# Optimization experiments

Measured on AMD Instinct MI355X. Metric: run time of the kernel, lower is better.

## Reference

```python
import jax, jax.numpy as jnp
import numpy as np

B, DIM, W = 16, 128, 16384
HEADS, DIM_HEAD = 4, 32
HIDDEN = HEADS * DIM_HEAD  # 128
SCALE = DIM_HEAD ** -0.5
EPS = 1e-5


def setup_inputs() -> dict:
    key = jax.random.key(0)
    k0, k1, k2, k3 = jax.random.split(key, 4)
    x = jax.random.normal(k0, (B, DIM, W), dtype=jnp.float32)
    # pointwise Conv1d weights (kernel_size=1) stored as [out_ch, in_ch]
    W_qkv = jax.random.normal(k1, (HIDDEN * 3, DIM), dtype=jnp.float32) * 0.02
    W_out = jax.random.normal(k2, (DIM, HIDDEN), dtype=jnp.float32) * 0.02
    b_out = jnp.zeros((DIM,), dtype=jnp.float32)
    gamma = jnp.ones((DIM,), dtype=jnp.float32)
    beta = jnp.zeros((DIM,), dtype=jnp.float32)
    return {"x": x, "W_qkv": W_qkv, "W_out": W_out, "b_out": b_out,
            "gamma": gamma, "beta": beta}


def reference(x, W_qkv, W_out, b_out, gamma, beta):
    b, c, w = x.shape
    # pointwise conv = channel matmul: (3*hidden, c) @ (b, c, w) -> (b, 3*hidden, w)
    qkv = jnp.einsum('oc,bcw->bow', W_qkv, x)
    q, k, v = jnp.split(qkv, 3, axis=1)
    rs = lambda t: t.reshape(b, HEADS, DIM_HEAD, w)  # b (h d) w -> b h d w
    q, k, v = rs(q), rs(k), rs(v)
    q = jax.nn.softmax(q, axis=-2) * SCALE   # softmax over head-dim d
    k = jax.nn.softmax(k, axis=-1)           # softmax over length n
    v = v / w
    # context: (b h d e) = sum_n k[b h d n] v[b h e n]
    context = jnp.einsum('bhdn,bhen->bhde', k, v)
    out = jnp.einsum('bhde,bhdn->bhen', context, q)  # (b h e n)
    out = out.reshape(b, HIDDEN, w)
    y = jnp.einsum('oc,bcw->bow', W_out, out) + b_out[None, :, None]
    # channel-wise LayerNorm over dim=1 (biased variance)
    mean = jnp.mean(y, axis=1, keepdims=True)
    var = jnp.var(y, axis=1, keepdims=True)
    y = (y - mean) * jax.lax.rsqrt(var + EPS)
    return y * gamma[None, :, None] + beta[None, :, None]
```

## Files before the change

### kernel.cpp

```cpp
#include <hip/hip_runtime.h>
#include <cstddef>

#define WLEN 16384
#define SCALEQ 0.17677669529663687f
#define CB_SCALE 16777216.0f
#define CB_INV   5.9604644775390625e-08f

typedef _Float16 half8 __attribute__((ext_vector_type(8)));
typedef _Float16 half4 __attribute__((ext_vector_type(4)));
typedef _Float16 half2v __attribute__((ext_vector_type(2)));
typedef float float4v __attribute__((ext_vector_type(4)));

#define WS_CTX 0
#define WS_DEN 65536
#define WS_WH  67584
#define WS_CB  92160

#define MFMA16(a, b, c) __builtin_amdgcn_mfma_f32_16x16x32_f16(a, b, c, 0, 0, 0)

__global__ __launch_bounds__(256) void k0_prep(const float* __restrict__ Wqkv,
                                               float* __restrict__ ws) {
  int idx = blockIdx.x * 256 + threadIdx.x;
  _Float16* Wh = (_Float16*)(ws + WS_WH);
  if (idx < 49152) Wh[idx] = (_Float16)Wqkv[idx];
}

__global__ __launch_bounds__(256, 2) void ka_ctx(
    const float* __restrict__ x, float* __restrict__ ws) {
  __shared__ __align__(16) _Float16 xh[32 * 136];
  __shared__ __align__(16) _Float16 ekl[4 * 32 * 40];
  __shared__ __align__(16) _Float16 vl[4 * 32 * 40];
  const int tid = threadIdx.x;
  const int lane = tid & 63, wv = tid >> 6;
  const int l15 = lane & 15, quad = lane >> 4;
  const int b = blockIdx.y, chunk = blockIdx.x;
  const _Float16* Wh = (const _Float16*)(ws + WS_WH);
  float* ctx = ws + WS_CTX;
  float* den = ws + WS_DEN;
  const float* xb = x + (size_t)b * 128 * WLEN;

  half8 afr[4][4];
  #pragma unroll
  for (int mt = 0; mt < 4; ++mt) {
    int row = (mt < 2) ? (128 + 32 * wv + mt * 16 + l15)
                       : (256 + 32 * wv + (mt - 2) * 16 + l15);
    #pragma unroll
    for (int ks = 0; ks < 4; ++ks)
      afr[mt][ks] = *(const half8*)(Wh + row * 128 + ks * 32 + quad * 8);
  }

  const float4v zero4 = {0.f, 0.f, 0.f, 0.f};
  float4v ctxa[2][2] = {zero4, zero4, zero4, zero4};
  float denr[8] = {0.f, 0.f, 0.f, 0.f, 0.f, 0.f, 0.f, 0.f};

  for (int s = 0; s < 16; ++s) {
    const int n0 = chunk * 512 + s * 32;
    __syncthreads();
    #pragma unroll
    for (int it = 0; it < 2; ++it) {
      int idx = it * 256 + tid;
      int f = idx & 7, cp = idx >> 3;
      const float* p0 = xb + (size_t)(2 * cp) * WLEN + n0 + 4 * f;
      float4 a = *(const float4*)p0;
      float4 c = *(const float4*)(p0 + WLEN);
      float av[4] = {a.x, a.y, a.z, a.w};
      float cv[4] = {c.x, c.y, c.z, c.w};
      #pragma unroll
      for (int i = 0; i < 4; ++i) {
        half2v h; h[0] = (_Float16)av[i]; h[1] = (_Float16)cv[i];
        *(half2v*)&xh[(4 * f + i) * 136 + 2 * cp] = h;
      }
    }
    __syncthreads();
    float4v acc[4][2] = {zero4, zero4, zero4, zero4, zero4, zero4, zero4, zero4};
    #pragma unroll
    for (int ks = 0; ks < 4; ++ks) {
      half8 b0 = *(const half8*)&xh[l15 * 136 + ks * 32 + quad * 8];
      half8 b1 = *(const half8*)&xh[(16 + l15) * 136 + ks * 32 + quad * 8];
      #pragma unroll
      for (int mt = 0; mt < 4; ++mt) {
        acc[mt][0] = MFMA16(afr[mt][ks], b0, acc[mt][0]);
        acc[mt][1] = MFMA16(afr[mt][ks], b1, acc[mt][1]);
      }
    }
    #pragma unroll
    for (int mt = 0; mt < 2; ++mt)
      #pragma unroll
      for (int nt = 0; nt < 2; ++nt)
        #pragma unroll
        for (int r = 0; r < 4; ++r) {
          float e = __expf(acc[mt][nt][r]);
          denr[mt * 4 + r] += e;
          ekl[(wv * 32 + mt * 16 + quad * 4 + r) * 40 + nt * 16 + l15] = (_Float16)e;
        }
    #pragma unroll
    for (int mt = 0; mt < 2; ++mt)
      #pragma unroll
      for (int nt = 0; nt < 2; ++nt)
        #pragma unroll
        for (int r = 0; r < 4; ++r)
          vl[(wv * 32 + mt * 16 + quad * 4 + r) * 40 + nt * 16 + l15] =
              (_Float16)acc[mt + 2][nt][r];
    half8 ae0 = *(const half8*)&ekl[(wv * 32 + l15) * 40 + quad * 8];
    half8 ae1 = *(const half8*)&ekl[(wv * 32 + 16 + l15) * 40 + quad * 8];
    half8 bv0 = *(const half8*)&vl[(wv * 32 + l15) * 40 + quad * 8];
    half8 bv1 = *(const half8*)&vl[(wv * 32 + 16 + l15) * 40 + quad * 8];
    ctxa[0][0] = MFMA16(ae0, bv0, ctxa[0][0]);
    ctxa[0][1] = MFMA16(ae0, bv1, ctxa[0][1]);
    ctxa[1][0] = MFMA16(ae1, bv0, ctxa[1][0]);
    ctxa[1][1] = MFMA16(ae1, bv1, ctxa[1][1]);
  }
  #pragma unroll
  for (int dt = 0; dt < 2; ++dt)
    #pragma unroll
    for (int et = 0; et < 2; ++et)
      #pragma unroll
      for (int r = 0; r < 4; ++r)
        atomicAdd(&ctx[((b * 4 + wv) * 32 + dt * 16 + quad * 4 + r) * 32 +
                       et * 16 + l15],
                  ctxa[dt][et][r]);
  #pragma unroll
  for (int i = 0; i < 8; ++i) {
    float v = denr[i];
    v += __shfl_xor(v, 1, 64);
    v += __shfl_xor(v, 2, 64);
    v += __shfl_xor(v, 4, 64);
    v += __shfl_xor(v, 8, 64);
    if (l15 == 0)
      atomicAdd(&den[(b * 4 + wv) * 32 + (i >> 2) * 16 + quad * 4 + (i & 3)], v);
  }
}

__global__ __launch_bounds__(256) void kb_cb(
    const float* __restrict__ Wout, float* __restrict__ ws) {
  __shared__ __align__(16) float nc[4096];
  const int b = blockIdx.x, tid = threadIdx.x;
  const float* ctx = ws + WS_CTX;
  const float* den = ws + WS_DEN;
  _Float16* cb = (_Float16*)(ws + WS_CB) + b * 16384;
  for (int i = tid; i < 4096; i += 256)
    nc[i] = ctx[b * 4096 + i] / (den[b * 128 + (i >> 5)] * 16384.0f);
  __syncthreads();
  const int o = tid >> 1, dh = (tid & 1) * 16;
  for (int h = 0; h < 4; ++h) {
    float wrow[32];
    #pragma unroll
    for (int e4 = 0; e4 < 8; ++e4) {
      float4 w4 = *(const float4*)(Wout + o * 128 + h * 32 + e4 * 4);
      wrow[e4 * 4 + 0] = w4.x; wrow[e4 * 4 + 1] = w4.y;
      wrow[e4 * 4 + 2] = w4.z; wrow[e4 * 4 + 3] = w4.w;
    }
    for (int d = 0; d < 16; ++d) {
      const float* ncr = &nc[(h * 32 + dh + d) * 32];
      float acc = 0.f;
      #pragma unroll
      for (int e = 0; e < 32; ++e) acc += wrow[e] * ncr[e];
      cb[o * 128 + h * 32 + dh + d] = (_Float16)(acc * CB_SCALE);
    }
  }
}

__global__ __launch_bounds__(256, 2) void kc_out(
    const float* __restrict__ x, const float* __restrict__ wsc,
    const float* __restrict__ b_out, const float* __restrict__ gamma,
    const float* __restrict__ beta, float* __restrict__ out) {
  __shared__ __align__(16) _Float16 xh[128 * 136];
  __shared__ float ssum[4][128], ssq[4][128];
  __shared__ float smean[128], sinv[128];
  const int tid = threadIdx.x;
  const int lane = tid & 63, wv = tid >> 6;
  const int l15 = lane & 15, quad = lane >> 4;
  const int b = blockIdx.y, tile = blockIdx.x;
  const int n0 = tile * 128;
  const _Float16* Wh = (const _Float16*)(wsc + WS_WH);
  const _Float16* cb = (const _Float16*)(wsc + WS_CB) + b * 16384;
  const float* xb = x + (size_t)b * 128 * WLEN;
  const float4v zero4 = {0.f, 0.f, 0.f, 0.f};

  half8 a1[2][4];
  #pragma unroll
  for (int mt = 0; mt < 2; ++mt)
    #pragma unroll
    for (int ks = 0; ks < 4; ++ks)
      a1[mt][ks] = *(const half8*)(Wh + (32 * wv + mt * 16 + l15) * 128 +
                                   ks * 32 + quad * 8);

  #pragma unroll
  for (int it = 0; it < 8; ++it) {
    int idx = it * 256 + tid;
    int f = (idx & 7) | ((idx >> 9) << 3);
    int cp = (idx >> 3) & 63;
    const float* p0 = xb + (size_t)(2 * cp) * WLEN + n0 + 4 * f;
    float4 a = *(const float4*)p0;
    float4 c = *(const float4*)(p0 + WLEN);
    float av[4] = {a.x, a.y, a.z, a.w};
    float cv[4] = {c.x, c.y, c.z, c.w};
    #pragma unroll
    for (int i = 0; i < 4; ++i) {
      half2v h; h[0] = (_Float16)av[i]; h[1] = (_Float16)cv[i];
      *(half2v*)&xh[(4 * f + i) * 136 + 2 * cp] = h;
    }
  }
  __syncthreads();

  float4v acc[2][8] = {zero4, zero4, zero4, zero4, zero4, zero4, zero4, zero4,
                       zero4, zero4, zero4, zero4, zero4, zero4, zero4, zero4};
  #pragma unroll
  for (int ks = 0; ks < 4; ++ks) {
    half8 bf[8];
    #pragma unroll
    for (int nt = 0; nt < 8; ++nt)
      bf[nt] = *(const half8*)&xh[(nt * 16 + l15) * 136 + ks * 32 + quad * 8];
    #pragma unroll
    for (int mt = 0; mt < 2; ++mt)
      #pragma unroll
      for (int nt = 0; nt < 8; ++nt)
        acc[mt][nt] = MFMA16(a1[mt][ks], bf[nt], acc[mt][nt]);
  }
  #pragma unroll
  for (int nt = 0; nt < 8; ++nt) {
    float mx = -1e30f;
    #pragma unroll
    for (int mt = 0; mt < 2; ++mt)
      #pragma unroll
      for (int r = 0; r < 4; ++r) mx = fmaxf(mx, acc[mt][nt][r]);
    mx = fmaxf(mx, __shfl_xor(mx, 16, 64));
    mx = fmaxf(mx, __shfl_xor(mx, 32, 64));
    float sm = 0.f;
    #pragma unroll
    for (int mt = 0; mt < 2; ++mt)
      #pragma unroll
      for (int r = 0; r < 4; ++r) {
        float e = __expf(acc[mt][nt][r] - mx);
        acc[mt][nt][r] = e;
        sm += e;
      }
    sm += __shfl_xor(sm, 16, 64);
    sm += __shfl_xor(sm, 32, 64);
    float sc = SCALEQ / sm;
    #pragma unroll
    for (int mt = 0; mt < 2; ++mt)
      #pragma unroll
      for (int r = 0; r < 4; ++r) acc[mt][nt][r] *= sc;
  }
  __syncthreads();
  #pragma unroll
  for (int mt = 0; mt < 2; ++mt)
    #pragma unroll
    for (int nt = 0; nt < 8; ++nt) {
      half4 hq;
      #pragma unroll
      for (int r = 0; r < 4; ++r) hq[r] = (_Float16)acc[mt][nt][r];
      *(half4*)&xh[(nt * 16 + l15) * 136 + 32 * wv + mt * 16 + quad * 4] = hq;
    }
  __syncthreads();

  half8 a2[2][4];
  #pragma unroll
  for (int mt = 0; mt < 2; ++mt)
    #pragma unroll
    for (int ks = 0; ks < 4; ++ks)
      a2[mt][ks] = *(const half8*)(cb + (32 * wv + mt * 16 + l15) * 128 +
                                   ks * 32 + quad * 8);
  float4v acc2[2][8] = {zero4, zero4, zero4, zero4, zero4, zero4, zero4, zero4,
                        zero4, zero4, zero4, zero4, zero4, zero4, zero4, zero4};
  #pragma unroll
  for (int ks = 0; ks < 4; ++ks) {
    half8 bf[8];
    #pragma unroll
    for (int nt = 0; nt < 8; ++nt)
      bf[nt] = *(const half8*)&xh[(nt * 16 + l15) * 136 + ks * 32 + quad * 8];
    #pragma unroll
    for (int mt = 0; mt < 2; ++mt)
      #pragma unroll
      for (int nt = 0; nt < 8; ++nt)
        acc2[mt][nt] = MFMA16(a2[mt][ks], bf[nt], acc2[mt][nt]);
  }

  float bo[8], ga[8], be[8];
  #pragma unroll
  for (int mt = 0; mt < 2; ++mt)
    #pragma unroll
    for (int r = 0; r < 4; ++r) {
      int o = 32 * wv + mt * 16 + quad * 4 + r;
      bo[mt * 4 + r] = b_out[o];
      ga[mt * 4 + r] = gamma[o];
      be[mt * 4 + r] = beta[o];
    }
  #pragma unroll
  for (int nt = 0; nt < 8; ++nt) {
    float ps = 0.f, pq = 0.f;
    #pragma unroll
    for (int mt = 0; mt < 2; ++mt)
      #pragma unroll
      for (int r = 0; r < 4; ++r) {
        float v = acc2[mt][nt][r] * CB_INV + bo[mt * 4 + r];
        acc2[mt][nt][r] = v;
        ps += v;
        pq += v * v;
      }
    ps += __shfl_xor(ps, 16, 64);
    ps += __shfl_xor(ps, 32, 64);
    pq += __shfl_xor(pq, 16, 64);
    pq += __shfl_xor(pq, 32, 64);
    if (quad == 0) {
      ssum[wv][nt * 16 + l15] = ps;
      ssq[wv][nt * 16 + l15] = pq;
    }
  }
  __syncthreads();
  if (tid < 128) {
    float s = ssum[0][tid] + ssum[1][tid] + ssum[2][tid] + ssum[3][tid];
    float q2 = ssq[0][tid] + ssq[1][tid] + ssq[2][tid] + ssq[3][tid];
    float mean = s * (1.0f / 128.0f);
    float var = q2 * (1.0f / 128.0f) - mean * mean;
    smean[tid] = mean;
    sinv[tid] = rsqrtf(var + 1e-5f);
  }
  __syncthreads();
  float* ob = out + (size_t)b * 128 * WLEN + n0;
  #pragma unroll
  for (int nt = 0; nt < 8; ++nt) {
    int n = nt * 16 + l15;
    float mean = smean[n], inv = sinv[n];
    #pragma unroll
    for (int mt = 0; mt < 2; ++mt)
      #pragma unroll
      for (int r = 0; r < 4; ++r) {
        int o = 32 * wv + mt * 16 + quad * 4 + r;
        ob[(size_t)o * WLEN + n] =
            (acc2[mt][nt][r] - mean) * inv * ga[mt * 4 + r] + be[mt * 4 + r];
      }
  }
}

extern "C" void kernel_launch(void* const* d_in, const int* in_sizes, int n_in,
                              void* d_out, int out_size, void* d_ws, size_t ws_size,
                              hipStream_t stream) {
  const float* x    = (const float*)d_in[0];
  const float* Wqkv = (const float*)d_in[1];
  const float* Wout = (const float*)d_in[2];
  const float* bo   = (const float*)d_in[3];
  const float* gam  = (const float*)d_in[4];
  const float* bet  = (const float*)d_in[5];
  float* out = (float*)d_out;
  float* ws  = (float*)d_ws;

  hipMemsetAsync(ws, 0, (65536 + 2048) * sizeof(float), stream);
  hipLaunchKernelGGL(k0_prep, dim3(192), dim3(256), 0, stream, Wqkv, ws);
  hipLaunchKernelGGL(ka_ctx, dim3(32, 16), dim3(256), 0, stream, x, ws);
  hipLaunchKernelGGL(kb_cb, dim3(16), dim3(256), 0, stream, Wout, ws);
  hipLaunchKernelGGL(kc_out, dim3(128, 16), dim3(256), 0, stream,
                     x, ws, bo, gam, bet, out);
}
```

Measured before the change: 302.9 us.

## Double-buffer x tiles in context kernel, fold weight conversion, split cb by head

Removes the separate fp16 weight-conversion kernel; the ka_ctx and kc_out kernels now load fp32 Wqkv and convert it in registers. In ka_ctx the x staging becomes double-buffered: the next tile's global loads are issued before the MFMA work on the current tile and written to the other LDS buffer afterward, dropping one barrier per iteration. kb_cb is split across heads in a 16x4 grid for more parallelism. The cost is more registers and LDS in ka_ctx, plus redundant fp32 weight loads per block.

```diff
diff --git a/kernel.cpp b/kernel.cpp
--- a/kernel.cpp
+++ b/kernel.cpp
@@ -13,28 +13,29 @@
 
 #define WS_CTX 0
 #define WS_DEN 65536
-#define WS_WH  67584
-#define WS_CB  92160
+#define WS_CB  67584
 
 #define MFMA16(a, b, c) __builtin_amdgcn_mfma_f32_16x16x32_f16(a, b, c, 0, 0, 0)
 
-__global__ __launch_bounds__(256) void k0_prep(const float* __restrict__ Wqkv,
-                                               float* __restrict__ ws) {
-  int idx = blockIdx.x * 256 + threadIdx.x;
-  _Float16* Wh = (_Float16*)(ws + WS_WH);
-  if (idx < 49152) Wh[idx] = (_Float16)Wqkv[idx];
+__device__ __forceinline__ half8 cvt8(float4 w0, float4 w1) {
+  half8 h;
+  h[0] = (_Float16)w0.x; h[1] = (_Float16)w0.y;
+  h[2] = (_Float16)w0.z; h[3] = (_Float16)w0.w;
+  h[4] = (_Float16)w1.x; h[5] = (_Float16)w1.y;
+  h[6] = (_Float16)w1.z; h[7] = (_Float16)w1.w;
+  return h;
 }
 
 __global__ __launch_bounds__(256, 2) void ka_ctx(
-    const float* __restrict__ x, float* __restrict__ ws) {
-  __shared__ __align__(16) _Float16 xh[32 * 136];
+    const float* __restrict__ x, const float* __restrict__ Wqkv,
+    float* __restrict__ ws) {
+  __shared__ __align__(16) _Float16 xh[2][32 * 136];
   __shared__ __align__(16) _Float16 ekl[4 * 32 * 40];
   __shared__ __align__(16) _Float16 vl[4 * 32 * 40];
   const int tid = threadIdx.x;
   const int lane = tid & 63, wv = tid >> 6;
   const int l15 = lane & 15, quad = lane >> 4;
   const int b = blockIdx.y, chunk = blockIdx.x;
-  const _Float16* Wh = (const _Float16*)(ws + WS_WH);
   float* ctx = ws + WS_CTX;
   float* den = ws + WS_DEN;
   const float* xb = x + (size_t)b * 128 * WLEN;
@@ -45,38 +46,54 @@
     int row = (mt < 2) ? (128 + 32 * wv + mt * 16 + l15)
                        : (256 + 32 * wv + (mt - 2) * 16 + l15);
     #pragma unroll
-    for (int ks = 0; ks < 4; ++ks)
-      afr[mt][ks] = *(const half8*)(Wh + row * 128 + ks * 32 + quad * 8);
-  }
+    for (int ks = 0; ks < 4; ++ks) {
+      const float* wp = Wqkv + row * 128 + ks * 32 + quad * 8;
+      afr[mt][ks] = cvt8(*(const float4*)wp, *(const float4*)(wp + 4));
+    }
+  }
+
+  const int f0 = tid & 7;
+  const int cp0 = tid >> 3;
+  const int cp1 = cp0 + 32;
+  float4 pa0, pc0, pa1, pc1;
+
+  auto LOADT = [&](int s) {
+    const float* base = xb + chunk * 512 + s * 32 + 4 * f0;
+    pa0 = *(const float4*)(base + (size_t)(2 * cp0) * WLEN);
+    pc0 = *(const float4*)(base + (size_t)(2 * cp0 + 1) * WLEN);
+    pa1 = *(const float4*)(base + (size_t)(2 * cp1) * WLEN);
+    pc1 = *(const float4*)(base + (size_t)(2 * cp1 + 1) * WLEN);
+  };
+  auto CVTW = [&](int bsel) {
+    _Float16* xd = xh[bsel];
+    float av0[4] = {pa0.x, pa0.y, pa0.z, pa0.w};
+    float cv0[4] = {pc0.x, pc0.y, pc0.z, pc0.w};
+    float av1[4] = {pa1.x, pa1.y, pa1.z, pa1.w};
+    float cv1[4] = {pc1.x, pc1.y, pc1.z, pc1.w};
+    #pragma unroll
+    for (int i = 0; i < 4; ++i) {
+      half2v h0; h0[0] = (_Float16)av0[i]; h0[1] = (_Float16)cv0[i];
+      *(half2v*)&xd[(4 * f0 + i) * 136 + 2 * cp0] = h0;
+      half2v h1; h1[0] = (_Float16)av1[i]; h1[1] = (_Float16)cv1[i];
+      *(half2v*)&xd[(4 * f0 + i) * 136 + 2 * cp1] = h1;
+    }
+  };
 
   const float4v zero4 = {0.f, 0.f, 0.f, 0.f};
   float4v ctxa[2][2] = {zero4, zero4, zero4, zero4};
   float denr[8] = {0.f, 0.f, 0.f, 0.f, 0.f, 0.f, 0.f, 0.f};
 
+  LOADT(0);
+  CVTW(0);
   for (int s = 0; s < 16; ++s) {
-    const int n0 = chunk * 512 + s * 32;
     __syncthreads();
-    #pragma unroll
-    for (int it = 0; it < 2; ++it) {
-      int idx = it * 256 + tid;
-      int f = idx & 7, cp = idx >> 3;
-      const float* p0 = xb + (size_t)(2 * cp) * WLEN + n0 + 4 * f;
-      float4 a = *(const float4*)p0;
-      float4 c = *(const float4*)(p0 + WLEN);
-      float av[4] = {a.x, a.y, a.z, a.w};
-      float cv[4] = {c.x, c.y, c.z, c.w};
-      #pragma unroll
-      for (int i = 0; i < 4; ++i) {
-        half2v h; h[0] = (_Float16)av[i]; h[1] = (_Float16)cv[i];
-        *(half2v*)&xh[(4 * f + i) * 136 + 2 * cp] = h;
-      }
-    }
-    __syncthreads();
+    if (s < 15) LOADT(s + 1);
+    const _Float16* xc = xh[s & 1];
     float4v acc[4][2] = {zero4, zero4, zero4, zero4, zero4, zero4, zero4, zero4};
     #pragma unroll
     for (int ks = 0; ks < 4; ++ks) {
-      half8 b0 = *(const half8*)&xh[l15 * 136 + ks * 32 + quad * 8];
-      half8 b1 = *(const half8*)&xh[(16 + l15) * 136 + ks * 32 + quad * 8];
+      half8 b0 = *(const half8*)&xc[l15 * 136 + ks * 32 + quad * 8];
+      half8 b1 = *(const half8*)&xc[(16 + l15) * 136 + ks * 32 + quad * 8];
       #pragma unroll
       for (int mt = 0; mt < 4; ++mt) {
         acc[mt][0] = MFMA16(afr[mt][ks], b0, acc[mt][0]);
@@ -109,6 +126,7 @@
     ctxa[0][1] = MFMA16(ae0, bv1, ctxa[0][1]);
     ctxa[1][0] = MFMA16(ae1, bv0, ctxa[1][0]);
     ctxa[1][1] = MFMA16(ae1, bv1, ctxa[1][1]);
+    if (s < 15) CVTW((s + 1) & 1);
   }
   #pragma unroll
   for (int dt = 0; dt < 2; ++dt)
@@ -133,37 +151,39 @@
 
 __global__ __launch_bounds__(256) void kb_cb(
     const float* __restrict__ Wout, float* __restrict__ ws) {
-  __shared__ __align__(16) float nc[4096];
-  const int b = blockIdx.x, tid = threadIdx.x;
+  __shared__ float nc[1024];
+  const int b = blockIdx.x, h = blockIdx.y, tid = threadIdx.x;
   const float* ctx = ws + WS_CTX;
   const float* den = ws + WS_DEN;
   _Float16* cb = (_Float16*)(ws + WS_CB) + b * 16384;
-  for (int i = tid; i < 4096; i += 256)
-    nc[i] = ctx[b * 4096 + i] / (den[b * 128 + (i >> 5)] * 16384.0f);
+  for (int i = tid; i < 1024; i += 256) {
+    int d = i >> 5;
+    nc[i] = ctx[((b * 4 + h) * 32 + d) * 32 + (i & 31)] /
+            (den[(b * 4 + h) * 32 + d] * 16384.0f);
+  }
   __syncthreads();
   const int o = tid >> 1, dh = (tid & 1) * 16;
-  for (int h = 0; h < 4; ++h) {
-    float wrow[32];
-    #pragma unroll
-    for (int e4 = 0; e4 < 8; ++e4) {
-      float4 w4 = *(const float4*)(Wout + o * 128 + h * 32 + e4 * 4);
-      wrow[e4 * 4 + 0] = w4.x; wrow[e4 * 4 + 1] = w4.y;
-      wrow[e4 * 4 + 2] = w4.z; wrow[e4 * 4 + 3] = w4.w;
-    }
-    for (int d = 0; d < 16; ++d) {
-      const float* ncr = &nc[(h * 32 + dh + d) * 32];
-      float acc = 0.f;
-      #pragma unroll
-      for (int e = 0; e < 32; ++e) acc += wrow[e] * ncr[e];
-      cb[o * 128 + h * 32 + dh + d] = (_Float16)(acc * CB_SCALE);
-    }
+  float wrow[32];
+  #pragma unroll
+  for (int e4 = 0; e4 < 8; ++e4) {
+    float4 w4 = *(const float4*)(Wout + o * 128 + h * 32 + e4 * 4);
+    wrow[e4 * 4 + 0] = w4.x; wrow[e4 * 4 + 1] = w4.y;
+    wrow[e4 * 4 + 2] = w4.z; wrow[e4 * 4 + 3] = w4.w;
+  }
+  for (int d = 0; d < 16; ++d) {
+    const float* ncr = &nc[(dh + d) * 32];
+    float acc = 0.f;
+    #pragma unroll
+    for (int e = 0; e < 32; ++e) acc += wrow[e] * ncr[e];
+    cb[o * 128 + h * 32 + dh + d] = (_Float16)(acc * CB_SCALE);
   }
 }
 
 __global__ __launch_bounds__(256, 2) void kc_out(
-    const float* __restrict__ x, const float* __restrict__ wsc,
-    const float* __restrict__ b_out, const float* __restrict__ gamma,
-    const float* __restrict__ beta, float* __restrict__ out) {
+    const float* __restrict__ x, const float* __restrict__ Wqkv,
+    const float* __restrict__ wsc, const float* __restrict__ b_out,
+    const float* __restrict__ gamma, const float* __restrict__ beta,
+    float* __restrict__ out) {
   __shared__ __align__(16) _Float16 xh[128 * 136];
   __shared__ float ssum[4][128], ssq[4][128];
   __shared__ float smean[128], sinv[128];
@@ -172,7 +192,6 @@
   const int l15 = lane & 15, quad = lane >> 4;
   const int b = blockIdx.y, tile = blockIdx.x;
   const int n0 = tile * 128;
-  const _Float16* Wh = (const _Float16*)(wsc + WS_WH);
   const _Float16* cb = (const _Float16*)(wsc + WS_CB) + b * 16384;
   const float* xb = x + (size_t)b * 128 * WLEN;
   const float4v zero4 = {0.f, 0.f, 0.f, 0.f};
@@ -181,9 +200,10 @@
   #pragma unroll
   for (int mt = 0; mt < 2; ++mt)
     #pragma unroll
-    for (int ks = 0; ks < 4; ++ks)
-      a1[mt][ks] = *(const half8*)(Wh + (32 * wv + mt * 16 + l15) * 128 +
-                                   ks * 32 + quad * 8);
+    for (int ks = 0; ks < 4; ++ks) {
+      const float* wp = Wqkv + (32 * wv + mt * 16 + l15) * 128 + ks * 32 + quad * 8;
+      a1[mt][ks] = cvt8(*(const float4*)wp, *(const float4*)(wp + 4));
+    }
 
   #pragma unroll
   for (int it = 0; it < 8; ++it) {
@@ -347,9 +367,8 @@
   float* ws  = (float*)d_ws;
 
   hipMemsetAsync(ws, 0, (65536 + 2048) * sizeof(float), stream);
-  hipLaunchKernelGGL(k0_prep, dim3(192), dim3(256), 0, stream, Wqkv, ws);
-  hipLaunchKernelGGL(ka_ctx, dim3(32, 16), dim3(256), 0, stream, x, ws);
-  hipLaunchKernelGGL(kb_cb, dim3(16), dim3(256), 0, stream, Wout, ws);
+  hipLaunchKernelGGL(ka_ctx, dim3(32, 16), dim3(256), 0, stream, x, Wqkv, ws);
+  hipLaunchKernelGGL(kb_cb, dim3(16, 4), dim3(256), 0, stream, Wout, ws);
   hipLaunchKernelGGL(kc_out, dim3(128, 16), dim3(256), 0, stream,
-                     x, ws, bo, gam, bet, out);
-}
+                     x, Wqkv, ws, bo, gam, bet, out);
+}
```

Result: faster. 295.0 us, median of 2 (-2.6%).
